# Optimization experiments

Measured on AMD Instinct MI355X. Metric: run time of the kernel, lower is better.

The kernel has to match this reference:

```python
import jax, jax.numpy as jnp
import numpy as np

DIM = 1024
NUM_HEADS = 16
HEAD_DIM = 64
EPS = 1e-6

def setup_inputs() -> dict:
    key = jax.random.key(0)
    ks = jax.random.split(key, 6)
    x = jax.random.normal(ks[0], (4, 2048, DIM), dtype=jnp.float32)
    # Linear weights stored as (in, out); torch nn.Linear computes x @ W.T with W (out,in),
    # equivalent math with our (in,out) layout.
    Wq = jax.random.normal(ks[1], (DIM, NUM_HEADS * HEAD_DIM), dtype=jnp.float32) / np.sqrt(DIM)
    Wk = jax.random.normal(ks[2], (DIM, NUM_HEADS * HEAD_DIM), dtype=jnp.float32) / np.sqrt(DIM)
    Wv = jax.random.normal(ks[3], (DIM, NUM_HEADS * HEAD_DIM), dtype=jnp.float32) / np.sqrt(DIM)
    Wo = jax.random.normal(ks[4], (NUM_HEADS * HEAD_DIM, DIM), dtype=jnp.float32) / np.sqrt(NUM_HEADS * HEAD_DIM)
    # FeatureMap buffer: randn(head_dim, head_dim)/sqrt(head_dim)
    proj = jax.random.normal(ks[5], (HEAD_DIM, HEAD_DIM), dtype=jnp.float32) / np.sqrt(HEAD_DIM)
    return {"x": x, "Wq": Wq, "Wk": Wk, "Wv": Wv, "Wo": Wo, "proj": proj}

def _feature_map(x, proj):
    # phi(x) = elu(x @ proj) + 1  (positive features)
    return jax.nn.elu(x @ proj) + 1.0

def reference(x, Wq, Wk, Wv, Wo, proj):
    B, S, _ = x.shape
    H, D = NUM_HEADS, HEAD_DIM
    q = (x @ Wq).reshape(B, S, H, D)
    k = (x @ Wk).reshape(B, S, H, D)
    v = (x @ Wv).reshape(B, S, H, D)
    q = _feature_map(q, proj)
    k = _feature_map(k, proj)
    # scan over time: carry kv_state (B,H,D,D) and k_state (B,H,D)
    q_t = jnp.moveaxis(q, 1, 0)  # (S,B,H,D)
    k_t = jnp.moveaxis(k, 1, 0)
    v_t = jnp.moveaxis(v, 1, 0)

    def step(carry, qkv):
        kv, ksum = carry
        qt, kt, vt = qkv  # each (B,H,D)
        kv = kv + kt[..., :, None] * vt[..., None, :]  # outer product k v^T
        ksum = ksum + kt
        num = jnp.einsum('bhd,bhde->bhe', qt, kv)
        den = jnp.einsum('bhd,bhd->bh', qt, ksum) + EPS
        return (kv, ksum), num / den[..., None]

    kv0 = jnp.zeros((B, H, D, D), dtype=x.dtype)
    ks0 = jnp.zeros((B, H, D), dtype=x.dtype)
    _, out = jax.lax.scan(step, (kv0, ks0), (q_t, k_t, v_t))
    out = jnp.moveaxis(out, 0, 1).reshape(B, S, H * D)  # (B,S,H*D)
    return out @ Wo
```

## Files before the change

kernel.cpp:

```cpp
#include <hip/hip_runtime.h>

typedef unsigned short u16;
typedef unsigned int   u32;
typedef short bfrag8 __attribute__((ext_vector_type(8)));
typedef float facc4  __attribute__((ext_vector_type(4)));

#define DIM    1024
#define NH     16
#define HD     64
#define BSZ    4
#define SEQ    2048
#define MROWS  (BSZ*SEQ)
#define CHUNK  64
#define NCHUNK (SEQ/CHUNK)
#define BH     (BSZ*NH)
#define TS     72
#define NT     16

__device__ __forceinline__ u16 f2bf(float f) {
  u32 u = __builtin_bit_cast(u32, f);
  u32 r = u + 0x7fffu + ((u >> 16) & 1u);
  return (u16)(r >> 16);
}
__device__ __forceinline__ float bf2f(u16 b) {
  return __builtin_bit_cast(float, (u32)b << 16);
}

__device__ __forceinline__ void gload_lds16(const void* g, void* l) {
  __builtin_amdgcn_global_load_lds((const __attribute__((address_space(1))) u32*)g,
                                   (__attribute__((address_space(3))) u32*)l, 16, 0, 0);
}

__global__ __launch_bounds__(256) void prep(const float* __restrict__ x,
                                            const float* __restrict__ Wq, const float* __restrict__ Wk,
                                            const float* __restrict__ Wv, const float* __restrict__ Wo,
                                            const float* __restrict__ proj,
                                            u16* __restrict__ xb, u16* __restrict__ wt) {
  __shared__ float smem[6144];
  const int bx = blockIdx.x, tid = threadIdx.x;
  if (bx < 8192) {
    const int i = (bx * 256 + tid) * 4;
    const float4 v = *(const float4*)(x + i);
    ushort4 o;
    o.x = f2bf(v.x); o.y = f2bf(v.y); o.z = f2bf(v.z); o.w = f2bf(v.w);
    *(ushort4*)(xb + i) = o;
  } else if (bx < 9216) {
    const int idx = bx - 8192;
    const int i0 = (idx & 31) * 32;
    const int h  = (idx >> 5) & 15;
    const int sel = idx >> 9;
    const float* W = sel ? Wk : Wq;
    u16* out = wt + (size_t)sel * (DIM*DIM);
    float* sp = smem;
    float* sw = smem + 4096;
    for (int s = tid; s < 4096; s += 256) sp[s] = proj[s];
    for (int s = tid; s < 2048; s += 256) {
      int r = s >> 6, c = s & 63;
      sw[s] = W[(size_t)(i0 + r)*DIM + h*64 + c];
    }
    __syncthreads();
    const int i  = tid >> 3;
    const int e0 = (tid & 7) * 8;
    #pragma unroll
    for (int ee = 0; ee < 8; ++ee) {
      const int e = e0 + ee;
      float acc = 0.f;
      for (int d = 0; d < 64; ++d) acc += sw[i*64 + d] * sp[d*64 + e];
      out[(size_t)(h*64 + e)*DIM + i0 + i] = f2bf(acc);
    }
  } else {
    const int idx = bx - 9216;
    const int n0 = (idx & 31) * 32;
    const int k0 = ((idx >> 5) & 31) * 32;
    const int sel = idx >> 10;
    const float* in = sel ? Wo : Wv;
    u16* out = wt + (size_t)(2 + sel) * (DIM*DIM);
    float* tile = smem;
    for (int s = tid; s < 1024; s += 256) {
      int r = s >> 5, c = s & 31;
      tile[r*33 + c] = in[(size_t)(k0 + r)*DIM + n0 + c];
    }
    __syncthreads();
    for (int s = tid; s < 1024; s += 256) {
      int r = s >> 5, c = s & 31;
      out[(size_t)(n0 + r)*DIM + k0 + c] = f2bf(tile[c*33 + r]);
    }
  }
}

#define SBAR0() __builtin_amdgcn_sched_barrier(0)

#define STAGE6(kt, bp) { \
  const int rih = tid >> 3, sl = tid & 7; \
  const int gc = ((sl ^ (rih & 7)) << 3); \
  _Pragma("unroll") for (int seg = 0; seg < 2; ++seg) \
    gload_lds16(A + (size_t)(m0 + seg*64 + rih)*DIM + (kt)*64 + gc, (bp) + seg*4096 + tid*8); \
  _Pragma("unroll") for (int seg = 0; seg < 4; ++seg) \
    gload_lds16(W + (size_t)(ngl + seg*64 + rih)*DIM + (kt)*64 + gc, (bp) + 8192 + seg*4096 + tid*8); \
}

#define RD8(xd, wd, bp, KH) { \
  _Pragma("unroll") for (int mf = 0; mf < 4; ++mf) { \
    const int row = wm*64 + mf*16 + lr; \
    xd[mf] = *(const bfrag8*)&(bp)[row*64 + ((((KH)*4+g) ^ (row & 7)) << 3)]; } \
  _Pragma("unroll") for (int nf = 0; nf < 4; ++nf) { \
    const int row = wn*64 + nf*16 + lr; \
    wd[nf] = *(const bfrag8*)&(bp)[8192 + row*64 + ((((KH)*4+g) ^ (row & 7)) << 3)]; } \
}

#define MM16(xs, ws) { __builtin_amdgcn_s_setprio(1); \
  _Pragma("unroll") for (int nf = 0; nf < 4; ++nf) \
    _Pragma("unroll") for (int mf = 0; mf < 4; ++mf) \
      acc[nf][mf] = __builtin_amdgcn_mfma_f32_16x16x32_bf16(ws[nf], xs[mf], acc[nf][mf], 0, 0, 0); \
  __builtin_amdgcn_s_setprio(0); }

template<int MODE>
__global__ __launch_bounds__(512, 1)
void gemmK(const u16* __restrict__ A, const u16* __restrict__ W,
           u16* __restrict__ outb, float* __restrict__ outf) {
  __shared__ u16 lds[2*24576];
  const int tid  = threadIdx.x;
  const int wave = tid >> 6, lane = tid & 63;
  const int wm = wave >> 2, wn = wave & 3;
  const int lr = lane & 15, g = lane >> 4;

  const int NY  = (MODE == 0) ? 12 : 4;
  const int q   = (int)gridDim.x >> 3;
  const int bid = (int)blockIdx.x;
  const int nf_ = (bid & 7) * q + (bid >> 3);
  const int m0  = (nf_ / NY) * 128;
  const int ngl = (nf_ % NY) * 256;

  STAGE6(0, lds);
  STAGE6(1, lds + 24576);
  asm volatile("s_waitcnt vmcnt(6)" ::: "memory");
  asm volatile("s_barrier" ::: "memory");

  facc4 acc[4][4] = {};
  bfrag8 xa[4], wa[4], xb[4], wb[4];

  RD8(xa, wa, lds, 0);

  #pragma unroll 2
  for (int t = 0; t < NT; ++t) {
    u16* bufp = lds + (t & 1) * 24576;
    u16* bufq = lds + ((t + 1) & 1) * 24576;
    asm volatile("s_waitcnt lgkmcnt(0)" ::: "memory"); SBAR0();
    RD8(xb, wb, bufp, 1);
    SBAR0();
    MM16(xa, wa);
    SBAR0();
    asm volatile("s_waitcnt vmcnt(0)" ::: "memory");
    asm volatile("s_barrier" ::: "memory");
    asm volatile("s_waitcnt lgkmcnt(0)" ::: "memory"); SBAR0();
    if (t + 2 < NT) STAGE6(t + 2, bufp);
    if (t + 1 < NT) RD8(xa, wa, bufq, 0);
    SBAR0();
    MM16(xb, wb);
    SBAR0();
    asm volatile("s_barrier" ::: "memory");
  }

  const int sel = (MODE == 0) ? (ngl >> 10) : 0;
  const bool doElu = (MODE == 0) && (sel < 2);
  const int coly = (MODE == 0) ? (ngl & 1023) : ngl;
  #pragma unroll
  for (int nf = 0; nf < 4; ++nf) {
    #pragma unroll
    for (int mf = 0; mf < 4; ++mf) {
      const facc4 a = acc[nf][mf];
      const int m = m0 + wm*64 + mf*16 + lr;
      const int col0 = coly + wn*64 + nf*16 + g*4;
      float v0 = a[0], v1 = a[1], v2 = a[2], v3 = a[3];
      if (MODE == 0) {
        if (doElu) {
          v0 = (v0 > 0.f) ? (v0 + 1.f) : __expf(v0);
          v1 = (v1 > 0.f) ? (v1 + 1.f) : __expf(v1);
          v2 = (v2 > 0.f) ? (v2 + 1.f) : __expf(v2);
          v3 = (v3 > 0.f) ? (v3 + 1.f) : __expf(v3);
        }
        uint2 pk;
        pk.x = (u32)f2bf(v0) | ((u32)f2bf(v1) << 16);
        pk.y = (u32)f2bf(v2) | ((u32)f2bf(v3) << 16);
        *(uint2*)&outb[(size_t)sel*((size_t)MROWS*DIM) + (size_t)m*DIM + col0] = pk;
      } else {
        float4 pk; pk.x = v0; pk.y = v1; pk.z = v2; pk.w = v3;
        *(float4*)&outf[(size_t)m*DIM + col0] = pk;
      }
    }
  }
}


__global__ __launch_bounds__(256) void phaseA(const u16* __restrict__ Kb, const u16* __restrict__ Vb,
                                              u16* __restrict__ Ast, float* __restrict__ ksum) {
  const int c = blockIdx.x, bh = blockIdx.y;
  const int b = bh >> 4, h = bh & 15;
  const int tid = threadIdx.x;
  const int wave = tid >> 6, lane = tid & 63, lr = lane & 15, g = lane >> 4;
  __shared__ u16 lKt[64*TS];
  __shared__ u16 lVt[64*TS];
  const size_t mbase = (size_t)b*SEQ + (size_t)c*CHUNK;

  for (int s = tid; s < 512; s += 256) {
    const int t = s >> 3, dg = (s & 7) * 8;
    const bfrag8 kk = *(const bfrag8*)&Kb[(mbase + t)*DIM + h*64 + dg];
    const bfrag8 vv = *(const bfrag8*)&Vb[(mbase + t)*DIM + h*64 + dg];
    #pragma unroll
    for (int j = 0; j < 8; ++j) {
      lKt[(dg + j)*TS + t] = (u16)kk[j];
      lVt[(dg + j)*TS + t] = (u16)vv[j];
    }
  }
  __syncthreads();

  facc4 acc[4] = {};
  #pragma unroll
  for (int kt = 0; kt < 2; ++kt) {
    const bfrag8 af = *(const bfrag8*)&lVt[(wave*16 + lr)*TS + kt*32 + g*8];
    #pragma unroll
    for (int j = 0; j < 4; ++j) {
      const bfrag8 bk = *(const bfrag8*)&lKt[(j*16 + lr)*TS + kt*32 + g*8];
      acc[j] = __builtin_amdgcn_mfma_f32_16x16x32_bf16(af, bk, acc[j], 0, 0, 0);
    }
  }
  u16* dst = Ast + (((size_t)bh*NCHUNK + c) << 12);
  #pragma unroll
  for (int j = 0; j < 4; ++j)
    #pragma unroll
    for (int r = 0; r < 4; ++r)
      dst[(wave*16 + g*4 + r)*64 + j*16 + lr] = f2bf(acc[j][r]);

  const int d = tid >> 2, seg = tid & 3;
  const bfrag8 k0 = *(const bfrag8*)&lKt[d*TS + seg*16];
  const bfrag8 k1 = *(const bfrag8*)&lKt[d*TS + seg*16 + 8];
  float s = 0.f;
  #pragma unroll
  for (int j = 0; j < 8; ++j) s += bf2f((u16)k0[j]) + bf2f((u16)k1[j]);
  s += __shfl_xor(s, 1, 64);
  s += __shfl_xor(s, 2, 64);
  if (seg == 0) ksum[((size_t)bh*NCHUNK + c)*64 + d] = s;
}

__global__ __launch_bounds__(256) void phaseB(u16* __restrict__ Ast, float* __restrict__ ksum) {
  const int bh = blockIdx.x, slice = blockIdx.y;
  const int tid = threadIdx.x;
  u16* base = Ast + (size_t)bh*NCHUNK*4096 + slice*256 + tid;
  float v[NCHUNK];
  #pragma unroll
  for (int c = 0; c < NCHUNK; ++c) v[c] = bf2f(base[(size_t)c*4096]);
  float run = 0.f;
  #pragma unroll
  for (int c = 0; c < NCHUNK; ++c) { base[(size_t)c*4096] = f2bf(run); run += v[c]; }
  if (slice == 0 && tid < 64) {
    float rs = 0.f;
    float* kp = ksum + (size_t)bh*NCHUNK*64 + tid;
    for (int c = 0; c < NCHUNK; ++c) { const float t = kp[c*64]; kp[c*64] = rs; rs += t; }
  }
}

__global__ __launch_bounds__(256) void phaseC(const u16* __restrict__ Qb, const u16* __restrict__ Kb,
                                              const u16* __restrict__ Vb, const u16* __restrict__ Ast,
                                              const float* __restrict__ ksum, u16* __restrict__ Ob) {
  const int c = blockIdx.x, bh = blockIdx.y;
  const int b = bh >> 4, h = bh & 15;
  const int tid = threadIdx.x;
  const int wave = tid >> 6, lane = tid & 63, lr = lane & 15, g = lane >> 4;
  __shared__ u16 lS  [64*TS];
  __shared__ u16 lVt [64*TS];
  __shared__ u16 lKVt[64*TS];
  __shared__ float lks[64];
  __shared__ float lrs[64];
  __shared__ float lqk[64];
  const size_t mbase = (size_t)b*SEQ + (size_t)c*CHUNK;

  for (int s = tid; s < 512; s += 256) {
    const int t = s >> 3, dg = (s & 7) * 8;
    const bfrag8 vv = *(const bfrag8*)&Vb[(mbase + t)*DIM + h*64 + dg];
    #pragma unroll
    for (int j = 0; j < 8; ++j) lVt[(dg + j)*TS + t] = (u16)vv[j];
  }
  const u16* kvsrc = Ast + (((size_t)bh*NCHUNK + c) << 12);
  for (int s = tid; s < 512; s += 256) {
    const int e = s >> 3, dg = (s & 7) * 8;
    *(bfrag8*)&lKVt[e*TS + dg] = *(const bfrag8*)&kvsrc[e*64 + dg];
  }
  if (tid < 64) lks[tid] = ksum[((size_t)bh*NCHUNK + c)*64 + tid];

  bfrag8 qf[2], kf[4][2];
  {
    const u16* qrow = Qb + (mbase + wave*16 + lr)*DIM + h*64;
    qf[0] = *(const bfrag8*)&qrow[g*8];
    qf[1] = *(const bfrag8*)&qrow[32 + g*8];
  }
  #pragma unroll
  for (int j = 0; j < 4; ++j) {
    const u16* krow = Kb + (mbase + j*16 + lr)*DIM + h*64;
    kf[j][0] = *(const bfrag8*)&krow[g*8];
    kf[j][1] = *(const bfrag8*)&krow[32 + g*8];
  }

  facc4 accs[4] = {};
  #pragma unroll
  for (int kt = 0; kt < 2; ++kt)
    #pragma unroll
    for (int j = 0; j < 4; ++j)
      accs[j] = __builtin_amdgcn_mfma_f32_16x16x32_bf16(qf[kt], kf[j][kt], accs[j], 0, 0, 0);

  float rs[4] = {0.f, 0.f, 0.f, 0.f};
  #pragma unroll
  for (int j = 0; j < 4; ++j) {
    const int cc = j*16 + lr;
    #pragma unroll
    for (int r = 0; r < 4; ++r) {
      const int rr = wave*16 + g*4 + r;
      const float vS = (cc <= rr) ? accs[j][r] : 0.f;
      rs[r] += vS;
      lS[rr*TS + cc] = f2bf(vS);
    }
  }
  #pragma unroll
  for (int r = 0; r < 4; ++r) {
    float t = rs[r];
    t += __shfl_xor(t, 1, 64); t += __shfl_xor(t, 2, 64);
    t += __shfl_xor(t, 4, 64); t += __shfl_xor(t, 8, 64);
    if (lr == 0) lrs[wave*16 + g*4 + r] = t;
  }
  __syncthreads();

  {
    const u16* qr2 = Qb + (mbase + wave*16 + lr)*DIM + h*64 + g*16;
    const bfrag8 a0 = *(const bfrag8*)&qr2[0];
    const bfrag8 a1 = *(const bfrag8*)&qr2[8];
    float t = 0.f;
    #pragma unroll
    for (int j = 0; j < 8; ++j)
      t += bf2f((u16)a0[j]) * lks[g*16 + j] + bf2f((u16)a1[j]) * lks[g*16 + 8 + j];
    t += __shfl_xor(t, 16, 64);
    t += __shfl_xor(t, 32, 64);
    if (g == 0) lqk[wave*16 + lr] = t;
  }

  facc4 acco[4] = {};
  #pragma unroll
  for (int kt = 0; kt < 2; ++kt) {
    const bfrag8 sf = *(const bfrag8*)&lS[(wave*16 + lr)*TS + kt*32 + g*8];
    #pragma unroll
    for (int j = 0; j < 4; ++j) {
      const bfrag8 vf = *(const bfrag8*)&lVt[(j*16 + lr)*TS + kt*32 + g*8];
      acco[j] = __builtin_amdgcn_mfma_f32_16x16x32_bf16(sf, vf, acco[j], 0, 0, 0);
    }
  }
  #pragma unroll
  for (int kt = 0; kt < 2; ++kt)
    #pragma unroll
    for (int j = 0; j < 4; ++j) {
      const bfrag8 kvf = *(const bfrag8*)&lKVt[(j*16 + lr)*TS + kt*32 + g*8];
      acco[j] = __builtin_amdgcn_mfma_f32_16x16x32_bf16(qf[kt], kvf, acco[j], 0, 0, 0);
    }

  #pragma unroll
  for (int r = 0; r < 4; ++r) {
    const int rr = wave*16 + g*4 + r;
    const float rden = 1.0f / (lrs[rr] + lqk[rr] + 1e-6f);
    #pragma unroll
    for (int j = 0; j < 4; ++j)
      Ob[(mbase + rr)*DIM + h*64 + j*16 + lr] = f2bf(acco[j][r] * rden);
  }
}

extern "C" void kernel_launch(void* const* d_in, const int* in_sizes, int n_in,
                              void* d_out, int out_size, void* d_ws, size_t ws_size,
                              hipStream_t stream) {
  const float* x    = (const float*)d_in[0];
  const float* Wq   = (const float*)d_in[1];
  const float* Wk   = (const float*)d_in[2];
  const float* Wv   = (const float*)d_in[3];
  const float* Wo   = (const float*)d_in[4];
  const float* proj = (const float*)d_in[5];
  float* out = (float*)d_out;

  char* ws = (char*)d_ws;
  u16*   xb   = (u16*)  (ws);
  u16*   wt   = (u16*)  (ws + 16777216);
  u16*   qkv  = (u16*)  (ws + 25165824);
  u16*   Ob   = (u16*)  (ws + 75497472);
  u16*   Ast  = (u16*)  (ws + 92274688);
  float* ksum = (float*)(ws + 109051904);
  (void)ws_size; (void)in_sizes; (void)n_in; (void)out_size;

  prep<<<dim3(11264), 256, 0, stream>>>(x, Wq, Wk, Wv, Wo, proj, xb, wt);

  gemmK<0><<<dim3(64*12), 512, 0, stream>>>(xb, wt, qkv, nullptr);

  const u16* Qb = qkv;
  const u16* Kb = qkv + (size_t)MROWS*DIM;
  const u16* Vb = qkv + 2*(size_t)MROWS*DIM;

  phaseA<<<dim3(NCHUNK, BH), 256, 0, stream>>>(Kb, Vb, Ast, ksum);
  phaseB<<<dim3(BH, 16), 256, 0, stream>>>(Ast, ksum);
  phaseC<<<dim3(NCHUNK, BH), 256, 0, stream>>>(Qb, Kb, Vb, Ast, ksum, Ob);

  gemmK<1><<<dim3(64*4), 512, 0, stream>>>(Ob, wt + 3*(size_t)DIM*DIM, nullptr, out);
}
```

Baseline: 188.5 us.

## Store transposed V chunks in phaseA and read MFMA operands directly from global in phaseC

phaseA now writes its LDS-transposed V tile to a new workspace buffer laid out per chunk. phaseC drops its LDS staging of V, KV state and ksum, and loads MFMA B-fragments straight from global memory. It also reuses the Q fragments already held in registers for the denominator dot product instead of reloading Q. The aim is to cut LDS traffic, transpose work and one barrier in phaseC, at the cost of an extra global write in phaseA and uncoalesced-ish global fragment reads.

```diff
diff --git a/kernel.cpp b/kernel.cpp
--- a/kernel.cpp
+++ b/kernel.cpp
@@ -193,7 +193,8 @@
 
 
 __global__ __launch_bounds__(256) void phaseA(const u16* __restrict__ Kb, const u16* __restrict__ Vb,
-                                              u16* __restrict__ Ast, float* __restrict__ ksum) {
+                                              u16* __restrict__ Ast, float* __restrict__ ksum,
+                                              u16* __restrict__ Vt) {
   const int c = blockIdx.x, bh = blockIdx.y;
   const int b = bh >> 4, h = bh & 15;
   const int tid = threadIdx.x;
@@ -231,6 +232,12 @@
     for (int r = 0; r < 4; ++r)
       dst[(wave*16 + g*4 + r)*64 + j*16 + lr] = f2bf(acc[j][r]);
 
+  u16* vt = Vt + (((size_t)bh*NCHUNK + c) << 12);
+  for (int s = tid; s < 512; s += 256) {
+    const int e = s >> 3, tg = (s & 7) * 8;
+    *(bfrag8*)&vt[e*64 + tg] = *(const bfrag8*)&lVt[e*TS + tg];
+  }
+
   const int d = tid >> 2, seg = tid & 3;
   const bfrag8 k0 = *(const bfrag8*)&lKt[d*TS + seg*16];
   const bfrag8 k1 = *(const bfrag8*)&lKt[d*TS + seg*16 + 8];
@@ -260,32 +267,19 @@
 }
 
 __global__ __launch_bounds__(256) void phaseC(const u16* __restrict__ Qb, const u16* __restrict__ Kb,
-                                              const u16* __restrict__ Vb, const u16* __restrict__ Ast,
+                                              const u16* __restrict__ Vt, const u16* __restrict__ Ast,
                                               const float* __restrict__ ksum, u16* __restrict__ Ob) {
   const int c = blockIdx.x, bh = blockIdx.y;
   const int b = bh >> 4, h = bh & 15;
   const int tid = threadIdx.x;
   const int wave = tid >> 6, lane = tid & 63, lr = lane & 15, g = lane >> 4;
-  __shared__ u16 lS  [64*TS];
-  __shared__ u16 lVt [64*TS];
-  __shared__ u16 lKVt[64*TS];
-  __shared__ float lks[64];
+  __shared__ u16 lS[64*TS];
   __shared__ float lrs[64];
   __shared__ float lqk[64];
   const size_t mbase = (size_t)b*SEQ + (size_t)c*CHUNK;
-
-  for (int s = tid; s < 512; s += 256) {
-    const int t = s >> 3, dg = (s & 7) * 8;
-    const bfrag8 vv = *(const bfrag8*)&Vb[(mbase + t)*DIM + h*64 + dg];
-    #pragma unroll
-    for (int j = 0; j < 8; ++j) lVt[(dg + j)*TS + t] = (u16)vv[j];
-  }
   const u16* kvsrc = Ast + (((size_t)bh*NCHUNK + c) << 12);
-  for (int s = tid; s < 512; s += 256) {
-    const int e = s >> 3, dg = (s & 7) * 8;
-    *(bfrag8*)&lKVt[e*TS + dg] = *(const bfrag8*)&kvsrc[e*64 + dg];
-  }
-  if (tid < 64) lks[tid] = ksum[((size_t)bh*NCHUNK + c)*64 + tid];
+  const u16* vsrc  = Vt  + (((size_t)bh*NCHUNK + c) << 12);
+  const float* kp  = ksum + ((size_t)bh*NCHUNK + c)*64;
 
   bfrag8 qf[2], kf[4][2];
   {
@@ -326,16 +320,22 @@
     t += __shfl_xor(t, 4, 64); t += __shfl_xor(t, 8, 64);
     if (lr == 0) lrs[wave*16 + g*4 + r] = t;
   }
-  __syncthreads();
 
   {
-    const u16* qr2 = Qb + (mbase + wave*16 + lr)*DIM + h*64 + g*16;
-    const bfrag8 a0 = *(const bfrag8*)&qr2[0];
-    const bfrag8 a1 = *(const bfrag8*)&qr2[8];
+    float4 ka = *(const float4*)&kp[g*8];
+    float4 kb2 = *(const float4*)&kp[g*8 + 4];
+    float4 kc = *(const float4*)&kp[32 + g*8];
+    float4 kd = *(const float4*)&kp[32 + g*8 + 4];
+    const float* kaf = &ka.x; const float* kbf = &kb2.x;
+    const float* kcf = &kc.x; const float* kdf = &kd.x;
     float t = 0.f;
     #pragma unroll
-    for (int j = 0; j < 8; ++j)
-      t += bf2f((u16)a0[j]) * lks[g*16 + j] + bf2f((u16)a1[j]) * lks[g*16 + 8 + j];
+    for (int j = 0; j < 4; ++j) {
+      t += bf2f((u16)qf[0][j])     * kaf[j];
+      t += bf2f((u16)qf[0][4 + j]) * kbf[j];
+      t += bf2f((u16)qf[1][j])     * kcf[j];
+      t += bf2f((u16)qf[1][4 + j]) * kdf[j];
+    }
     t += __shfl_xor(t, 16, 64);
     t += __shfl_xor(t, 32, 64);
     if (g == 0) lqk[wave*16 + lr] = t;
@@ -347,7 +347,7 @@
     const bfrag8 sf = *(const bfrag8*)&lS[(wave*16 + lr)*TS + kt*32 + g*8];
     #pragma unroll
     for (int j = 0; j < 4; ++j) {
-      const bfrag8 vf = *(const bfrag8*)&lVt[(j*16 + lr)*TS + kt*32 + g*8];
+      const bfrag8 vf = *(const bfrag8*)&vsrc[(j*16 + lr)*64 + kt*32 + g*8];
       acco[j] = __builtin_amdgcn_mfma_f32_16x16x32_bf16(sf, vf, acco[j], 0, 0, 0);
     }
   }
@@ -355,7 +355,7 @@
   for (int kt = 0; kt < 2; ++kt)
     #pragma unroll
     for (int j = 0; j < 4; ++j) {
-      const bfrag8 kvf = *(const bfrag8*)&lKVt[(j*16 + lr)*TS + kt*32 + g*8];
+      const bfrag8 kvf = *(const bfrag8*)&kvsrc[(j*16 + lr)*64 + kt*32 + g*8];
       acco[j] = __builtin_amdgcn_mfma_f32_16x16x32_bf16(qf[kt], kvf, acco[j], 0, 0, 0);
     }
 
@@ -387,6 +387,7 @@
   u16*   Ob   = (u16*)  (ws + 75497472);
   u16*   Ast  = (u16*)  (ws + 92274688);
   float* ksum = (float*)(ws + 109051904);
+  u16*   Vt   = (u16*)  (ws + 109576192);
   (void)ws_size; (void)in_sizes; (void)n_in; (void)out_size;
 
   prep<<<dim3(11264), 256, 0, stream>>>(x, Wq, Wk, Wv, Wo, proj, xb, wt);
@@ -397,9 +398,9 @@
   const u16* Kb = qkv + (size_t)MROWS*DIM;
   const u16* Vb = qkv + 2*(size_t)MROWS*DIM;
 
-  phaseA<<<dim3(NCHUNK, BH), 256, 0, stream>>>(Kb, Vb, Ast, ksum);
+  phaseA<<<dim3(NCHUNK, BH), 256, 0, stream>>>(Kb, Vb, Ast, ksum, Vt);
   phaseB<<<dim3(BH, 16), 256, 0, stream>>>(Ast, ksum);
-  phaseC<<<dim3(NCHUNK, BH), 256, 0, stream>>>(Qb, Kb, Vb, Ast, ksum, Ob);
+  phaseC<<<dim3(NCHUNK, BH), 256, 0, stream>>>(Qb, Kb, Vt, Ast, ksum, Ob);
 
   gemmK<1><<<dim3(64*4), 512, 0, stream>>>(Ob, wt + 3*(size_t)DIM*DIM, nullptr, out);
 }
```

Measured after the change: 195.6 us. +3.8%, slower.

## Load activation fragments directly from global memory, stage only weights in LDS

Applied to the files above, without the earlier changes.

The GEMM kernel no longer stages the A (activation) tile through LDS. Each wave now loads its A MFMA fragments straight from global memory into registers, and only the weight tile is double-buffered in LDS, which shrinks the LDS footprint. The wait counts and barriers are reworked to overlap the direct global loads with the MFMAs. The trade-off is that A is fetched redundantly by the four wn waves per wm, with less coalesced 16-byte-per-lane global reads, in exchange for fewer LDS writes and less barrier traffic.

```diff
diff --git a/kernel.cpp b/kernel.cpp
--- a/kernel.cpp
+++ b/kernel.cpp
@@ -90,22 +90,22 @@
 
 #define SBAR0() __builtin_amdgcn_sched_barrier(0)
 
-#define STAGE6(kt, bp) { \
+#define STAGEW(kt, bp) { \
   const int rih = tid >> 3, sl = tid & 7; \
   const int gc = ((sl ^ (rih & 7)) << 3); \
-  _Pragma("unroll") for (int seg = 0; seg < 2; ++seg) \
-    gload_lds16(A + (size_t)(m0 + seg*64 + rih)*DIM + (kt)*64 + gc, (bp) + seg*4096 + tid*8); \
   _Pragma("unroll") for (int seg = 0; seg < 4; ++seg) \
-    gload_lds16(W + (size_t)(ngl + seg*64 + rih)*DIM + (kt)*64 + gc, (bp) + 8192 + seg*4096 + tid*8); \
-}
-
-#define RD8(xd, wd, bp, KH) { \
-  _Pragma("unroll") for (int mf = 0; mf < 4; ++mf) { \
-    const int row = wm*64 + mf*16 + lr; \
-    xd[mf] = *(const bfrag8*)&(bp)[row*64 + ((((KH)*4+g) ^ (row & 7)) << 3)]; } \
+    gload_lds16(W + (size_t)(ngl + seg*64 + rih)*DIM + (kt)*64 + gc, (bp) + seg*4096 + tid*8); \
+}
+
+#define RDWL(wd, bp, KH) { \
   _Pragma("unroll") for (int nf = 0; nf < 4; ++nf) { \
     const int row = wn*64 + nf*16 + lr; \
-    wd[nf] = *(const bfrag8*)&(bp)[8192 + row*64 + ((((KH)*4+g) ^ (row & 7)) << 3)]; } \
+    wd[nf] = *(const bfrag8*)&(bp)[row*64 + ((((KH)*4+g) ^ (row & 7)) << 3)]; } \
+}
+
+#define RDXG(xd, kt, KH) { \
+  _Pragma("unroll") for (int mf = 0; mf < 4; ++mf) { \
+    xd[mf] = *(const bfrag8*)&A[(size_t)(m0 + wm*64 + mf*16 + lr)*DIM + (kt)*64 + (KH)*32 + g*8]; } \
 }
 
 #define MM16(xs, ws) { __builtin_amdgcn_s_setprio(1); \
@@ -116,9 +116,9 @@
 
 template<int MODE>
 __global__ __launch_bounds__(512, 1)
-void gemmK(const u16* __restrict__ A, const u16* __restrict__ W,
+void gemmX(const u16* __restrict__ A, const u16* __restrict__ W,
            u16* __restrict__ outb, float* __restrict__ outf) {
-  __shared__ u16 lds[2*24576];
+  __shared__ u16 lds[2*16384];
   const int tid  = threadIdx.x;
   const int wave = tid >> 6, lane = tid & 63;
   const int wm = wave >> 2, wn = wave & 3;
@@ -131,34 +131,39 @@
   const int m0  = (nf_ / NY) * 128;
   const int ngl = (nf_ % NY) * 256;
 
-  STAGE6(0, lds);
-  STAGE6(1, lds + 24576);
-  asm volatile("s_waitcnt vmcnt(6)" ::: "memory");
-  asm volatile("s_barrier" ::: "memory");
-
   facc4 acc[4][4] = {};
   bfrag8 xa[4], wa[4], xb[4], wb[4];
 
-  RD8(xa, wa, lds, 0);
-
-  #pragma unroll 2
+  STAGEW(0, lds);
+  STAGEW(1, lds + 16384);
+  RDXG(xa, 0, 0);
+  SBAR0();
+  asm volatile("s_waitcnt vmcnt(8)" ::: "memory");
+  asm volatile("s_barrier" ::: "memory");
+  RDWL(wa, lds, 0);
+  SBAR0();
+
   for (int t = 0; t < NT; ++t) {
-    u16* bufp = lds + (t & 1) * 24576;
-    u16* bufq = lds + ((t + 1) & 1) * 24576;
-    asm volatile("s_waitcnt lgkmcnt(0)" ::: "memory"); SBAR0();
-    RD8(xb, wb, bufp, 1);
+    u16* bufp = lds + (t & 1) * 16384;
+    u16* bufq = lds + ((t + 1) & 1) * 16384;
+    RDWL(wb, bufp, 1);
+    RDXG(xb, t, 1);
+    SBAR0();
+    asm volatile("s_waitcnt vmcnt(4) lgkmcnt(4)" ::: "memory");
     SBAR0();
     MM16(xa, wa);
     SBAR0();
-    asm volatile("s_waitcnt vmcnt(0)" ::: "memory");
+    asm volatile("s_waitcnt lgkmcnt(0)" ::: "memory");
     asm volatile("s_barrier" ::: "memory");
-    asm volatile("s_waitcnt lgkmcnt(0)" ::: "memory"); SBAR0();
-    if (t + 2 < NT) STAGE6(t + 2, bufp);
-    if (t + 1 < NT) RD8(xa, wa, bufq, 0);
+    if (t + 2 < NT) STAGEW(t + 2, bufp);
+    if (t + 1 < NT) { RDWL(wa, bufq, 0); RDXG(xa, t + 1, 0); }
+    SBAR0();
+    if (t + 2 < NT)      asm volatile("s_waitcnt vmcnt(8) lgkmcnt(4)" ::: "memory");
+    else if (t + 1 < NT) asm volatile("s_waitcnt vmcnt(4) lgkmcnt(4)" ::: "memory");
+    else                 asm volatile("s_waitcnt vmcnt(0) lgkmcnt(0)" ::: "memory");
     SBAR0();
     MM16(xb, wb);
     SBAR0();
-    asm volatile("s_barrier" ::: "memory");
   }
 
   const int sel = (MODE == 0) ? (ngl >> 10) : 0;
@@ -391,7 +396,7 @@
 
   prep<<<dim3(11264), 256, 0, stream>>>(x, Wq, Wk, Wv, Wo, proj, xb, wt);
 
-  gemmK<0><<<dim3(64*12), 512, 0, stream>>>(xb, wt, qkv, nullptr);
+  gemmX<0><<<dim3(64*12), 512, 0, stream>>>(xb, wt, qkv, nullptr);
 
   const u16* Qb = qkv;
   const u16* Kb = qkv + (size_t)MROWS*DIM;
@@ -401,5 +406,5 @@
   phaseB<<<dim3(BH, 16), 256, 0, stream>>>(Ast, ksum);
   phaseC<<<dim3(NCHUNK, BH), 256, 0, stream>>>(Qb, Kb, Vb, Ast, ksum, Ob);
 
-  gemmK<1><<<dim3(64*4), 512, 0, stream>>>(Ob, wt + 3*(size_t)DIM*DIM, nullptr, out);
-}
+  gemmX<1><<<dim3(64*4), 512, 0, stream>>>(Ob, wt + 3*(size_t)DIM*DIM, nullptr, out);
+}
```

Result: slower. 271.6 us (+44.1%).
